# Kernel optimization log

Hardware: AMD Instinct MI355X
Metric: run time of the kernel (lower is better)

## Reference

```python
import jax, jax.numpy as jnp
import numpy as np

N = 4096   # nodes
D = 512    # feature dim
E = 65536  # edges
HOPS = 10  # APPNP K (init arg 'hops')
ALPHA = 0.5


def setup_inputs() -> dict:
    key = jax.random.key(0)
    k1, k2, k3 = jax.random.split(key, 3)
    x_train = jax.random.normal(k1, (N, D), dtype=jnp.float32)
    # kernel_scale = nn.Linear(D, 1, bias=False) weight, flattened to [D]
    w = jax.random.normal(k2, (D,), dtype=jnp.float32) * 0.05
    edge_index = jax.random.randint(k3, (2, E), 0, N, dtype=jnp.int32)
    return {"x_train": x_train, "w": w, "edge_index": edge_index}


def appnp(x0, src, dst, hops, alpha):
    # torch_geometric APPNP with gcn_norm (add self-loops, symmetric norm), dropout=0
    n = x0.shape[0]
    loop = jnp.arange(n, dtype=src.dtype)
    s = jnp.concatenate([src, loop])
    d = jnp.concatenate([dst, loop])
    deg = jax.ops.segment_sum(jnp.ones_like(s, dtype=x0.dtype), d, num_segments=n)
    dis = deg ** -0.5  # deg >= 1 thanks to self-loops
    norm = dis[s] * dis[d]

    def body(h, _):
        agg = jax.ops.segment_sum(norm[:, None] * h[s], d, num_segments=n)
        return (1.0 - alpha) * agg + alpha * x0, None

    h, _ = jax.lax.scan(body, x0, None, length=hops)
    return h


def reference(x_train, w, edge_index):
    n = x_train.shape[0]
    # RBF_kernel: K[i,j] = sum_d w_d * (x_i - x_j)_d^2 for i != j, diag = 1 (the eye)
    xw = x_train * w                                   # [N, D]
    sq = jnp.sum(xw * x_train, axis=1)                 # [N] weighted squared norms
    K = sq[:, None] + sq[None, :] - 2.0 * (xw @ x_train.T)  # [N, N]
    idx = jnp.arange(n)
    K = K.at[idx, idx].set(1.0)

    src, dst = edge_index[0], edge_index[1]
    kgg = appnp(K, src, dst, HOPS, ALPHA)
    kgg = appnp(kgg.T, src, dst, HOPS, ALPHA)

    # adj = dense coo(edge_index, ones); diag = (diag(adj.sum(dim=1)) + 1) ** -0.5
    # (adds 1 to the WHOLE matrix, so off-diagonal entries become 1.0 -- faithful)
    deg_row = jax.ops.segment_sum(jnp.ones((edge_index.shape[1],), K.dtype), src, num_segments=n)
    Dmat = (jnp.diag(deg_row) + 1.0) ** -0.5           # [N, N]
    kgg = Dmat * kgg       # elementwise, as in the original
    kgg = Dmat * kgg.T
    return kgg
```

## Files before the change

kernel.cpp:

```cpp
#include <hip/hip_runtime.h>
#include <stdint.h>

#define Nn 4096
#define Dd 512
#define Ee 65536
#define HOPS 10
#define TPB 512
#define RPT (Nn / TPB)
#define CT 4
#define WCAP 64
#define KEXT 1536
#define YC 640
#define XK 8192

typedef short bf16x8 __attribute__((ext_vector_type(8)));
typedef float f32x4 __attribute__((ext_vector_type(4)));

__device__ __forceinline__ unsigned short bf16r(float x) {
  unsigned int b = __float_as_uint(x);
  return (unsigned short)((b + 0x7FFFu + ((b >> 16) & 1u)) >> 16);
}
__device__ __forceinline__ float ubf(unsigned short h) {
  return __uint_as_float(((unsigned int)h) << 16);
}
__device__ __forceinline__ void gld16(const unsigned short* g, unsigned short* lds) {
  __builtin_amdgcn_global_load_lds(
      (const __attribute__((address_space(1))) unsigned int*)g,
      (__attribute__((address_space(3))) unsigned int*)lds, 16, 0, 0);
}

__global__ __launch_bounds__(256) void k_sq(const float* __restrict__ x,
                                            const float* __restrict__ w,
                                            float* __restrict__ sq) {
  int row = blockIdx.x;
  int tid = threadIdx.x;
  const float* xr = x + (size_t)row * Dd;
  float partial = 0.f;
  for (int d = tid; d < Dd; d += 256) {
    float xv = xr[d];
    partial += xv * xv * w[d];
  }
  for (int off = 32; off >= 1; off >>= 1) partial += __shfl_down(partial, off, 64);
  __shared__ float red[4];
  int wv = tid >> 6, ln = tid & 63;
  if (ln == 0) red[wv] = partial;
  __syncthreads();
  if (tid == 0) sq[row] = red[0] + red[1] + red[2] + red[3];
}

__global__ void k_count(const int* __restrict__ src, const int* __restrict__ dst,
                        int* __restrict__ degi, int* __restrict__ degrow) {
  int e = blockIdx.x * blockDim.x + threadIdx.x;
  if (e < Ee) {
    atomicAdd(&degi[dst[e]], 1);
    atomicAdd(&degrow[src[e]], 1);
  }
}

__global__ void k_dis(const int* __restrict__ degi, const int* __restrict__ degrow,
                      float* __restrict__ dis, float* __restrict__ d2) {
  int i = blockIdx.x * 256 + threadIdx.x;
  dis[i] = rsqrtf((float)(degi[i] + 1));
  d2[i] = 1.0f / ((float)degrow[i] + 1.0f);
}

__global__ void k_hist(const int* __restrict__ degi, int* __restrict__ binbase) {
  __shared__ int h[WCAP + 1];
  int t = threadIdx.x;
  if (t <= WCAP) h[t] = 0;
  __syncthreads();
  for (int i = t; i < Nn; i += 256) {
    int d = degi[i] + 1;
    if (d > WCAP) d = WCAP;
    atomicAdd(&h[d], 1);
  }
  __syncthreads();
  if (t == 0) {
    int run = 0;
    for (int b = 0; b <= WCAP; b++) { int c = h[b]; binbase[b] = run; run += c; }
  }
}

__global__ void k_scatter(const int* __restrict__ degi, const int* __restrict__ binbase,
                          int* __restrict__ bincnt, int* __restrict__ perm,
                          int* __restrict__ rnk) {
  int i = blockIdx.x * 256 + threadIdx.x;
  int d = degi[i] + 1;
  if (d > WCAP) d = WCAP;
  int pos = binbase[d] + atomicAdd(&bincnt[d], 1);
  perm[pos] = i;
  rnk[i] = pos;
}

__global__ void k_wsub(const int* __restrict__ degi, const int* __restrict__ perm,
                       int* __restrict__ wsub) {
  int t = threadIdx.x;
  int d = degi[perm[t * 64 + 63]] + 1;
  wsub[t] = d > WCAP ? WCAP : d;
}

__global__ void k_fill_ell(const int* __restrict__ src, const int* __restrict__ dst,
                           const float* __restrict__ dis, const int* __restrict__ rnk,
                           int* __restrict__ slot, int2* __restrict__ ell) {
  int i = blockIdx.x * blockDim.x + threadIdx.x;
  if (i < Ee) {
    int s = src[i], d = dst[i];
    int p = atomicAdd(&slot[d], 1);
    if (p < WCAP) ell[(size_t)p * Nn + rnk[d]] = make_int2(s, __float_as_int(dis[s] * dis[d]));
  } else if (i < Ee + Nn) {
    int v = i - Ee;
    int p = atomicAdd(&slot[v], 1);
    if (p < WCAP) ell[(size_t)p * Nn + rnk[v]] = make_int2(v, __float_as_int(dis[v] * dis[v]));
  }
}

__global__ __launch_bounds__(256) void k_xpose(const float* __restrict__ x,
                                               unsigned short* __restrict__ xb) {
  __shared__ float tile[32][33];
  int cx = blockIdx.x, rx = blockIdx.y;
  int t = threadIdx.x, txc = t & 31, tyc = t >> 5;
#pragma unroll
  for (int i = 0; i < 4; i++) {
    int a = tyc + i * 8;
    tile[a][txc] = x[(size_t)(rx * 32 + a) * Dd + cx * 32 + txc];
  }
  __syncthreads();
#pragma unroll
  for (int i = 0; i < 4; i++) {
    int a = tyc + i * 8;
    int c = cx * 32 + a;
    float v = tile[txc][a];
    unsigned short hi = bf16r(v);
    xb[(size_t)c * XK + rx * 32 + txc] = hi;
    xb[(size_t)c * XK + Nn + rx * 32 + txc] = bf16r(v - ubf(hi));
  }
}

__global__ void k_tail(const float* __restrict__ sq, unsigned short* __restrict__ xb) {
  int r = blockIdx.x * 256 + threadIdx.x;
  float v = sq[r];
  unsigned short hi = bf16r(v);
  xb[(size_t)512 * XK + r] = hi;
  xb[(size_t)512 * XK + Nn + r] = bf16r(v - ubf(hi));
  xb[(size_t)513 * XK + r] = bf16r(1.0f);
  xb[(size_t)513 * XK + Nn + r] = 0;
}

__global__ __launch_bounds__(TPB, 4) void k_appnp(unsigned short* __restrict__ mb,
                                                  const int2* __restrict__ ell,
                                                  const int* __restrict__ perm,
                                                  const int* __restrict__ wsub) {
  extern __shared__ float4 h4[];
  int j0 = blockIdx.x * CT;
  int tid = threadIdx.x;
  int wv = tid >> 6, ln = tid & 63;
  int qb = wv * 512 + ln;

#pragma unroll
  for (int rr = 0; rr < RPT; rr++) {
    int r = tid + rr * TPB;
    float4 v;
    v.x = (r == j0 + 0) ? 1.f : 0.f;
    v.y = (r == j0 + 1) ? 1.f : 0.f;
    v.z = (r == j0 + 2) ? 1.f : 0.f;
    v.w = (r == j0 + 3) ? 1.f : 0.f;
    h4[r] = v;
  }

  int ws[RPT];
#pragma unroll
  for (int rr = 0; rr < RPT; rr++)
    ws[rr] = __builtin_amdgcn_readfirstlane(wsub[wv * 8 + rr]);
  const int Wv = ws[RPT - 1];

  int rp[RPT];
#pragma unroll
  for (int rr = 0; rr < RPT; rr++) rp[rr] = perm[qb + rr * 64];

  __syncthreads();
  float4 x0r[RPT];
#pragma unroll
  for (int rr = 0; rr < RPT; rr++) x0r[rr] = h4[rp[rr]];

  float4 acc[RPT];
  for (int it = 0; it < HOPS; it++) {
    int2 cur[RPT];
#pragma unroll
    for (int rr = 0; rr < RPT; rr++) cur[rr] = ell[qb + rr * 64];
#pragma unroll
    for (int rr = 0; rr < RPT; rr++) acc[rr] = x0r[rr];
    for (int s = 0; s < Wv; s++) {
      int sn = s + 1;
      int2 nxt[RPT];
#pragma unroll
      for (int rr = 0; rr < RPT; rr++)
        if (sn < ws[rr]) nxt[rr] = ell[(size_t)sn * Nn + qb + rr * 64];
#pragma unroll
      for (int rr = 0; rr < RPT; rr++)
        if (s < ws[rr]) {
          float vv = __int_as_float(cur[rr].y);
          float4 hu = h4[cur[rr].x];
          acc[rr].x = fmaf(vv, hu.x, acc[rr].x);
          acc[rr].y = fmaf(vv, hu.y, acc[rr].y);
          acc[rr].z = fmaf(vv, hu.z, acc[rr].z);
          acc[rr].w = fmaf(vv, hu.w, acc[rr].w);
        }
#pragma unroll
      for (int rr = 0; rr < RPT; rr++)
        if (sn < ws[rr]) cur[rr] = nxt[rr];
    }
#pragma unroll
    for (int rr = 0; rr < RPT; rr++) {
      acc[rr].x *= 0.5f; acc[rr].y *= 0.5f; acc[rr].z *= 0.5f; acc[rr].w *= 0.5f;
    }
    __syncthreads();
#pragma unroll
    for (int rr = 0; rr < RPT; rr++) h4[rp[rr]] = acc[rr];
    __syncthreads();
  }

#pragma unroll
  for (int rr = 0; rr < RPT; rr++) {
    int r = tid + rr * TPB;
    float4 a = h4[r];
    ushort4 o = make_ushort4(bf16r(a.x), bf16r(a.y), bf16r(a.z), bf16r(a.w));
    *(ushort4*)&mb[(size_t)r * Nn + j0] = o;
  }
}

__device__ __forceinline__ void mm_step(const unsigned short* __restrict__ Ap, int lda,
                                        const unsigned short* __restrict__ Bp, int ldb,
                                        unsigned short* As, unsigned short* Bs,
                                        int i0, int j0, int k0, int l, int w, int wr,
                                        int wc, f32x4 acc[4][4]) {
  int rsub = w * 8 + (l >> 3);
  int scg = ((l & 7) ^ (l >> 3)) * 8;
#pragma unroll
  for (int r = 0; r < 4; r++) {
    int row = r * 32 + rsub;
    gld16(Ap + (size_t)(i0 + row) * lda + k0 + scg, As + (r * 32 + w * 8) * 64);
    gld16(Bp + (size_t)(j0 + row) * ldb + k0 + scg, Bs + (r * 32 + w * 8) * 64);
  }
  __syncthreads();
#pragma unroll
  for (int q = 0; q < 2; q++) {
    bf16x8 af[4], bg[4];
#pragma unroll
    for (int m = 0; m < 4; m++) {
      int ar = wr * 64 + m * 16 + (l & 15);
      af[m] = *(const bf16x8*)(As + ar * 64 + ((((l >> 4) + 4 * q) ^ (ar & 7)) * 8));
      int br = wc * 64 + m * 16 + (l & 15);
      bg[m] = *(const bf16x8*)(Bs + br * 64 + ((((l >> 4) + 4 * q) ^ (br & 7)) * 8));
    }
#pragma unroll
    for (int m = 0; m < 4; m++)
#pragma unroll
      for (int n = 0; n < 4; n++)
        acc[m][n] = __builtin_amdgcn_mfma_f32_16x16x32_bf16(af[m], bg[n], acc[m][n], 0, 0, 0);
  }
  __syncthreads();
}

__global__ __launch_bounds__(256) void k_ymm(const unsigned short* __restrict__ Mb,
                                             const unsigned short* __restrict__ xb,
                                             const float* __restrict__ wp,
                                             unsigned short* __restrict__ aext,
                                             unsigned short* __restrict__ bext,
                                             float* __restrict__ mu,
                                             float* __restrict__ m1) {
  __shared__ unsigned short As[128 * 64];
  __shared__ unsigned short Bs[128 * 64];
  int i0 = blockIdx.y * 128, j0 = blockIdx.x * 128;
  int tid = threadIdx.x, l = tid & 63, w = tid >> 6;
  int wr = w >> 1, wc = w & 1;
  f32x4 acc[4][4];
#pragma unroll
  for (int m = 0; m < 4; m++)
#pragma unroll
    for (int n = 0; n < 4; n++) acc[m][n] = (f32x4){0.f, 0.f, 0.f, 0.f};

  for (int k0 = 0; k0 < Nn; k0 += 64)
    mm_step(Mb, Nn, xb, XK, As, Bs, i0, j0, k0, l, w, wr, wc, acc);
  for (int k0 = 0; k0 < Nn; k0 += 64)
    mm_step(Mb, Nn, xb + Nn, XK, As, Bs, i0, j0, k0, l, w, wr, wc, acc);

#pragma unroll
  for (int m = 0; m < 4; m++) {
#pragma unroll
    for (int n = 0; n < 4; n++) {
#pragma unroll
      for (int q = 0; q < 4; q++) {
        int gi = i0 + wr * 64 + m * 16 + ((l >> 4) << 2) + q;
        int gj = j0 + wc * 64 + n * 16 + (l & 15);
        float y = acc[m][n][q];
        if (gj < 512) {
          unsigned short yhi = bf16r(y);
          unsigned short ylo = bf16r(y - ubf(yhi));
          float p = -2.f * wp[gj] * y;
          unsigned short phi = bf16r(p);
          unsigned short plo = bf16r(p - ubf(phi));
          bext[(size_t)gi * KEXT + gj] = yhi;
          bext[(size_t)gi * KEXT + 512 + gj] = ylo;
          bext[(size_t)gi * KEXT + 1024 + gj] = yhi;
          aext[(size_t)gi * KEXT + gj] = phi;
          aext[(size_t)gi * KEXT + 512 + gj] = phi;
          aext[(size_t)gi * KEXT + 1024 + gj] = plo;
        } else if (gj == 512) {
          mu[gi] = y;
        } else if (gj == 513) {
          m1[gi] = y;
        }
      }
    }
  }
}

__global__ __launch_bounds__(256) void k_mm(const unsigned short* __restrict__ Mb,
                                            const unsigned short* __restrict__ Aext,
                                            const unsigned short* __restrict__ Bext,
                                            const float* __restrict__ mu,
                                            const float* __restrict__ m1,
                                            const float* __restrict__ d2,
                                            float* __restrict__ out) {
  __shared__ unsigned short As[128 * 64];
  __shared__ unsigned short Bs[128 * 64];
  int lid = blockIdx.y * 32 + blockIdx.x;
  int swz = (lid & 7) * 128 + (lid >> 3);
  int i0 = (swz >> 5) * 128, j0 = (swz & 31) * 128;
  int tid = threadIdx.x, l = tid & 63, w = tid >> 6;
  int wr = w >> 1, wc = w & 1;
  f32x4 acc[4][4];
#pragma unroll
  for (int m = 0; m < 4; m++)
#pragma unroll
    for (int n = 0; n < 4; n++) acc[m][n] = (f32x4){0.f, 0.f, 0.f, 0.f};

  for (int k0 = 0; k0 < Nn; k0 += 64)
    mm_step(Mb, Nn, Mb, Nn, As, Bs, i0, j0, k0, l, w, wr, wc, acc);
  for (int k0 = 0; k0 < KEXT; k0 += 64)
    mm_step(Aext, KEXT, Bext, KEXT, As, Bs, i0, j0, k0, l, w, wr, wc, acc);

#pragma unroll
  for (int m = 0; m < 4; m++) {
#pragma unroll
    for (int n = 0; n < 4; n++) {
#pragma unroll
      for (int q = 0; q < 4; q++) {
        int gi = i0 + wr * 64 + m * 16 + ((l >> 4) << 2) + q;
        int gj = j0 + wc * 64 + n * 16 + (l & 15);
        float v = acc[m][n][q] + mu[gi] * m1[gj] + m1[gi] * mu[gj];
        if (gi == gj) v *= d2[gi];
        out[(size_t)gi * Nn + gj] = v;
      }
    }
  }
}

extern "C" void kernel_launch(void* const* d_in, const int* in_sizes, int n_in,
                              void* d_out, int out_size, void* d_ws, size_t ws_size,
                              hipStream_t stream) {
  const float* x = (const float*)d_in[0];
  const float* w = (const float*)d_in[1];
  const int* ei = (const int*)d_in[2];
  const int* src = ei;
  const int* dstv = ei + Ee;
  float* out = (float*)d_out;

  unsigned short* Mb = (unsigned short*)d_ws;
  unsigned short* aext = Mb + (size_t)Nn * Nn;
  unsigned short* bext = aext + (size_t)Nn * KEXT;
  unsigned short* xb = bext + (size_t)Nn * KEXT;
  int2* ell = (int2*)(xb + (size_t)YC * XK);
  float* sq = (float*)(ell + (size_t)WCAP * Nn);
  float* dis = sq + Nn;
  float* d2 = dis + Nn;
  float* mu = d2 + Nn;
  float* m1 = mu + Nn;
  int* degi = (int*)(m1 + Nn);
  int* degrow = degi + Nn;
  int* slotcnt = degrow + Nn;
  int* bincnt = slotcnt + Nn;
  int* binbase = bincnt + (WCAP + 1);
  int* perm = binbase + (WCAP + 1);
  int* rnk = perm + Nn;
  int* wsub = rnk + Nn;

  hipMemsetAsync(ell, 0, (size_t)WCAP * Nn * sizeof(int2), stream);
  hipMemsetAsync(degi, 0, sizeof(int) * (3 * Nn + (WCAP + 1)), stream);
  hipMemsetAsync(xb, 0, (size_t)YC * XK * sizeof(unsigned short), stream);

  k_sq<<<Nn, 256, 0, stream>>>(x, w, sq);
  k_count<<<Ee / 256, 256, 0, stream>>>(src, dstv, degi, degrow);
  k_dis<<<Nn / 256, 256, 0, stream>>>(degi, degrow, dis, d2);
  k_hist<<<1, 256, 0, stream>>>(degi, binbase);
  k_scatter<<<Nn / 256, 256, 0, stream>>>(degi, binbase, bincnt, perm, rnk);
  k_wsub<<<1, 64, 0, stream>>>(degi, perm, wsub);
  k_fill_ell<<<(Ee + Nn + 255) / 256, 256, 0, stream>>>(src, dstv, dis, rnk, slotcnt, ell);
  k_xpose<<<dim3(16, 128), 256, 0, stream>>>(x, xb);
  k_tail<<<Nn / 256, 256, 0, stream>>>(sq, xb);

  k_appnp<<<Nn / CT, TPB, Nn * sizeof(float4), stream>>>(Mb, ell, perm, wsub);
  k_ymm<<<dim3(YC / 128, Nn / 128), 256, 0, stream>>>(Mb, xb, w, aext, bext, mu, m1);
  k_mm<<<dim3(32, 32), 256, 0, stream>>>(Mb, aext, bext, mu, m1, d2, out);
}
```

Before: 908.3 us.

## Store APPNP propagation state as bf16 in LDS to process eight columns per block

The APPNP propagation kernel now keeps the hop state in shared memory as packed bf16 instead of fp32. Each 16-byte LDS gather therefore carries eight columns rather than four, which halves the number of blocks and the total edge/index reads across the grid. The x0 term is rebuilt from a column index rather than held in registers. The cost is rounding the state to bf16 at every hop, which adds error across the ten hops, plus more accumulator registers per thread.

```diff
diff --git a/kernel.cpp b/kernel.cpp
--- a/kernel.cpp
+++ b/kernel.cpp
@@ -7,7 +7,7 @@
 #define HOPS 10
 #define TPB 512
 #define RPT (Nn / TPB)
-#define CT 4
+#define CT8 8
 #define WCAP 64
 #define KEXT 1536
 #define YC 640
@@ -19,6 +19,9 @@
 __device__ __forceinline__ unsigned short bf16r(float x) {
   unsigned int b = __float_as_uint(x);
   return (unsigned short)((b + 0x7FFFu + ((b >> 16) & 1u)) >> 16);
+}
+__device__ __forceinline__ unsigned int pkbf(float lo, float hi) {
+  return (unsigned int)bf16r(lo) | ((unsigned int)bf16r(hi) << 16);
 }
 __device__ __forceinline__ float ubf(unsigned short h) {
   return __uint_as_float(((unsigned int)h) << 16);
@@ -150,8 +153,8 @@
                                                   const int2* __restrict__ ell,
                                                   const int* __restrict__ perm,
                                                   const int* __restrict__ wsub) {
-  extern __shared__ float4 h4[];
-  int j0 = blockIdx.x * CT;
+  extern __shared__ uint4 h4u[];
+  int j0 = blockIdx.x * CT8;
   int tid = threadIdx.x;
   int wv = tid >> 6, ln = tid & 63;
   int qb = wv * 512 + ln;
@@ -159,12 +162,16 @@
 #pragma unroll
   for (int rr = 0; rr < RPT; rr++) {
     int r = tid + rr * TPB;
-    float4 v;
-    v.x = (r == j0 + 0) ? 1.f : 0.f;
-    v.y = (r == j0 + 1) ? 1.f : 0.f;
-    v.z = (r == j0 + 2) ? 1.f : 0.f;
-    v.w = (r == j0 + 3) ? 1.f : 0.f;
-    h4[r] = v;
+    uint4 v = make_uint4(0u, 0u, 0u, 0u);
+    int c = r - j0;
+    if (c >= 0 && c < 8) {
+      unsigned int one = (c & 1) ? 0x3F800000u : 0x00003F80u;
+      if ((c >> 1) == 0) v.x = one;
+      else if ((c >> 1) == 1) v.y = one;
+      else if ((c >> 1) == 2) v.z = one;
+      else v.w = one;
+    }
+    h4u[r] = v;
   }
 
   int ws[RPT];
@@ -173,22 +180,24 @@
     ws[rr] = __builtin_amdgcn_readfirstlane(wsub[wv * 8 + rr]);
   const int Wv = ws[RPT - 1];
 
-  int rp[RPT];
-#pragma unroll
-  for (int rr = 0; rr < RPT; rr++) rp[rr] = perm[qb + rr * 64];
-
-  __syncthreads();
-  float4 x0r[RPT];
-#pragma unroll
-  for (int rr = 0; rr < RPT; rr++) x0r[rr] = h4[rp[rr]];
-
-  float4 acc[RPT];
+  int rp[RPT], x0c[RPT];
+#pragma unroll
+  for (int rr = 0; rr < RPT; rr++) {
+    rp[rr] = perm[qb + rr * 64];
+    int c = rp[rr] - j0;
+    x0c[rr] = (c >= 0 && c < 8) ? c : -1;
+  }
+  __syncthreads();
+
   for (int it = 0; it < HOPS; it++) {
     int2 cur[RPT];
 #pragma unroll
     for (int rr = 0; rr < RPT; rr++) cur[rr] = ell[qb + rr * 64];
-#pragma unroll
-    for (int rr = 0; rr < RPT; rr++) acc[rr] = x0r[rr];
+    float acc[RPT][8];
+#pragma unroll
+    for (int rr = 0; rr < RPT; rr++)
+#pragma unroll
+      for (int c = 0; c < 8; c++) acc[rr][c] = (x0c[rr] == c) ? 1.0f : 0.0f;
     for (int s = 0; s < Wv; s++) {
       int sn = s + 1;
       int2 nxt[RPT];
@@ -199,32 +208,37 @@
       for (int rr = 0; rr < RPT; rr++)
         if (s < ws[rr]) {
           float vv = __int_as_float(cur[rr].y);
-          float4 hu = h4[cur[rr].x];
-          acc[rr].x = fmaf(vv, hu.x, acc[rr].x);
-          acc[rr].y = fmaf(vv, hu.y, acc[rr].y);
-          acc[rr].z = fmaf(vv, hu.z, acc[rr].z);
-          acc[rr].w = fmaf(vv, hu.w, acc[rr].w);
+          uint4 hu = h4u[cur[rr].x];
+          acc[rr][0] = fmaf(vv, __uint_as_float(hu.x << 16), acc[rr][0]);
+          acc[rr][1] = fmaf(vv, __uint_as_float(hu.x & 0xFFFF0000u), acc[rr][1]);
+          acc[rr][2] = fmaf(vv, __uint_as_float(hu.y << 16), acc[rr][2]);
+          acc[rr][3] = fmaf(vv, __uint_as_float(hu.y & 0xFFFF0000u), acc[rr][3]);
+          acc[rr][4] = fmaf(vv, __uint_as_float(hu.z << 16), acc[rr][4]);
+          acc[rr][5] = fmaf(vv, __uint_as_float(hu.z & 0xFFFF0000u), acc[rr][5]);
+          acc[rr][6] = fmaf(vv, __uint_as_float(hu.w << 16), acc[rr][6]);
+          acc[rr][7] = fmaf(vv, __uint_as_float(hu.w & 0xFFFF0000u), acc[rr][7]);
         }
 #pragma unroll
       for (int rr = 0; rr < RPT; rr++)
         if (sn < ws[rr]) cur[rr] = nxt[rr];
     }
+    __syncthreads();
 #pragma unroll
     for (int rr = 0; rr < RPT; rr++) {
-      acc[rr].x *= 0.5f; acc[rr].y *= 0.5f; acc[rr].z *= 0.5f; acc[rr].w *= 0.5f;
-    }
-    __syncthreads();
-#pragma unroll
-    for (int rr = 0; rr < RPT; rr++) h4[rp[rr]] = acc[rr];
+      uint4 v;
+      v.x = pkbf(0.5f * acc[rr][0], 0.5f * acc[rr][1]);
+      v.y = pkbf(0.5f * acc[rr][2], 0.5f * acc[rr][3]);
+      v.z = pkbf(0.5f * acc[rr][4], 0.5f * acc[rr][5]);
+      v.w = pkbf(0.5f * acc[rr][6], 0.5f * acc[rr][7]);
+      h4u[rp[rr]] = v;
+    }
     __syncthreads();
   }
 
 #pragma unroll
   for (int rr = 0; rr < RPT; rr++) {
     int r = tid + rr * TPB;
-    float4 a = h4[r];
-    ushort4 o = make_ushort4(bf16r(a.x), bf16r(a.y), bf16r(a.z), bf16r(a.w));
-    *(ushort4*)&mb[(size_t)r * Nn + j0] = o;
+    *(uint4*)&mb[(size_t)r * Nn + j0] = h4u[r];
   }
 }
 
@@ -399,7 +413,7 @@
   k_xpose<<<dim3(16, 128), 256, 0, stream>>>(x, xb);
   k_tail<<<Nn / 256, 256, 0, stream>>>(sq, xb);
 
-  k_appnp<<<Nn / CT, TPB, Nn * sizeof(float4), stream>>>(Mb, ell, perm, wsub);
+  k_appnp<<<Nn / CT8, TPB, Nn * sizeof(uint4), stream>>>(Mb, ell, perm, wsub);
   k_ymm<<<dim3(YC / 128, Nn / 128), 256, 0, stream>>>(Mb, xb, w, aext, bext, mu, m1);
   k_mm<<<dim3(32, 32), 256, 0, stream>>>(Mb, aext, bext, mu, m1, d2, out);
 }
```

Result: no change. 891.7 us (-1.8%).
